# Performance work log

Measured on AMD Instinct MI355X. Metric: run time of the kernel, lower is better.

The kernel has to match this reference:

```python
import jax, jax.numpy as jnp
import numpy as np

INPUT_SIZE = 128
HID = 64
B, T = 256, 1024

def setup_inputs() -> dict:
    key = jax.random.key(0)
    ks = jax.random.split(key, 12)
    s1 = 1.0 / np.sqrt(HID)
    def u(k, shape):
        return jax.random.uniform(k, shape, jnp.float32, -s1, s1)
    return {
        "x": jax.random.normal(ks[0], (B, T, INPUT_SIZE), jnp.float32),
        "w_ih0": u(ks[1], (4 * HID, INPUT_SIZE)),
        "w_hh0": u(ks[2], (4 * HID, HID)),
        "b_ih0": u(ks[3], (4 * HID,)),
        "b_hh0": u(ks[4], (4 * HID,)),
        "w_ih1": u(ks[5], (4 * HID, HID)),
        "w_hh1": u(ks[6], (4 * HID, HID)),
        "b_ih1": u(ks[7], (4 * HID,)),
        "b_hh1": u(ks[8], (4 * HID,)),
        "w_out": u(ks[9], (1, HID)),
        "b_out": u(ks[10], (1,)),
    }

def _lstm(x, w_ih, w_hh, b_ih, b_hh):
    # x: [B, T, I] -> h sequence [B, T, H]; PyTorch gate order i, f, g, o
    Bb = x.shape[0]
    H = w_hh.shape[1]
    # precompute input contribution for all timesteps (one big GEMM)
    xg = jnp.einsum('bti,gi->btg', x, w_ih) + b_ih + b_hh  # [B, T, 4H]
    def step(carry, g_t):
        h, c = carry
        g = g_t + h @ w_hh.T  # [B, 4H]
        i, f, gg, o = jnp.split(g, 4, axis=-1)
        i = jax.nn.sigmoid(i)
        f = jax.nn.sigmoid(f)
        gg = jnp.tanh(gg)
        o = jax.nn.sigmoid(o)
        c = f * c + i * gg
        h = o * jnp.tanh(c)
        return (h, c), h
    init = (jnp.zeros((Bb, H), x.dtype), jnp.zeros((Bb, H), x.dtype))
    _, hs = jax.lax.scan(step, init, jnp.swapaxes(xg, 0, 1))  # [T, B, H]
    return jnp.swapaxes(hs, 0, 1)

def reference(x, w_ih0, w_hh0, b_ih0, b_hh0, w_ih1, w_hh1, b_ih1, b_hh1, w_out, b_out):
    h1 = _lstm(x, w_ih0, w_hh0, b_ih0, b_hh0)   # [B, T, H]
    h2 = _lstm(h1, w_ih1, w_hh1, b_ih1, b_hh1)  # [B, T, H]
    logits = jnp.einsum('bth,oh->bto', h2, w_out) + b_out  # [B, T, 1]
    return jax.nn.sigmoid(logits)
```

## Files before the change

kernel.cpp:

```cpp
#include <hip/hip_runtime.h>

#define BB 256
#define TT 1024
#define II 128
#define HH 64
#define BT (BB * TT)

typedef _Float16 h2 __attribute__((ext_vector_type(2)));
typedef _Float16 half8 __attribute__((ext_vector_type(8)));
typedef float f32x4 __attribute__((ext_vector_type(4)));
typedef unsigned int uint;
typedef unsigned short ushort;

#define DOT2(a, b, c) __builtin_amdgcn_fdot2((a), (b), (c), false)
#define BC(u) __builtin_bit_cast(h2, (uint)(u))
#define MFMA16(a, b, c) __builtin_amdgcn_mfma_f32_16x16x32_f16((a), (b), (c), 0, 0, 0)
#define SIG(v) __builtin_amdgcn_rcpf(1.0f + __expf(-(v)))
#define TNH(v) (1.0f - 2.0f * __builtin_amdgcn_rcpf(1.0f + __expf(2.0f * (v))))

#define BAR_W8() asm volatile("s_waitcnt lgkmcnt(8)\n\ts_barrier" ::: "memory")
#define BAR_W0() asm volatile("s_waitcnt lgkmcnt(0)\n\ts_barrier" ::: "memory")
#define BAR_NP() asm volatile("s_barrier" ::: "memory")

#define LDPK(P, ptr) uint P; { float2 _f = *(const float2*)(ptr); \
    h2 _h; _h[0] = (_Float16)_f.x; _h[1] = (_Float16)_f.y; \
    P = __builtin_bit_cast(uint, _h); }
#define PIN8(a,b,c,d,e,f,g,h_) asm volatile("" : "+v"(a),"+v"(b),"+v"(c),"+v"(d),"+v"(e),"+v"(f),"+v"(g),"+v"(h_));
#define LD8(P, base, o) \
    LDPK(P##0,(base)+(o)+ 0) LDPK(P##1,(base)+(o)+ 2) LDPK(P##2,(base)+(o)+ 4) LDPK(P##3,(base)+(o)+ 6) \
    LDPK(P##4,(base)+(o)+ 8) LDPK(P##5,(base)+(o)+10) LDPK(P##6,(base)+(o)+12) LDPK(P##7,(base)+(o)+14) \
    PIN8(P##0,P##1,P##2,P##3,P##4,P##5,P##6,P##7)

#define D8A(P, va, vb, c0, c1, c2, c3) \
    c0 = DOT2(BC(P##0), BC((va).x), c0); c1 = DOT2(BC(P##1), BC((va).y), c1); \
    c2 = DOT2(BC(P##2), BC((va).z), c2); c3 = DOT2(BC(P##3), BC((va).w), c3); \
    c0 = DOT2(BC(P##4), BC((vb).x), c0); c1 = DOT2(BC(P##5), BC((vb).y), c1); \
    c2 = DOT2(BC(P##6), BC((vb).z), c2); c3 = DOT2(BC(P##7), BC((vb).w), c3);

#define GDOT(G, s) { float a0=0.f,a1=0.f,a2=0.f,a3=0.f; \
    D8A(G##A, hv0, hv1, a0,a1,a2,a3) D8A(G##B, hv2, hv3, a0,a1,a2,a3) \
    D8A(G##C, hv4, hv5, a0,a1,a2,a3) D8A(G##D, hv6, hv7, a0,a1,a2,a3) \
    s = (a0 + a1) + (a2 + a3); }

#define LDHV(src) { const uint4* hq_ = (const uint4*)(src); \
    hv0=hq_[0]; hv1=hq_[1]; hv2=hq_[2]; hv3=hq_[3]; \
    hv4=hq_[4]; hv5=hq_[5]; hv6=hq_[6]; hv7=hq_[7]; }

__global__ __launch_bounds__(256)
void xg_mfma(const float* __restrict__ x, const float* __restrict__ w_ih0,
             ushort* __restrict__ xg)
{
    __shared__ __align__(16) _Float16 xt[64][136];
    __shared__ __align__(16) _Float16 wt[128][136];
    const int tid = threadIdx.x, lane = tid & 63, wv = tid >> 6;
    const int bt0 = blockIdx.x * 64;
    {
        const int row = tid >> 2, q = (tid & 3) * 32;
        const float4* src = (const float4*)(x + (size_t)(bt0 + row) * II + q);
        _Float16* dst = &xt[row][q];
        #pragma unroll
        for (int i = 0; i < 8; ++i) {
            float4 v = src[i];
            dst[4*i+0]=(_Float16)v.x; dst[4*i+1]=(_Float16)v.y;
            dst[4*i+2]=(_Float16)v.z; dst[4*i+3]=(_Float16)v.w;
        }
    }
    for (int nh = 0; nh < 2; ++nh) {
        __syncthreads();
        {
            const int n = tid >> 1, kh = (tid & 1) * 64;
            const int flatn = nh * 128 + n;
            const int srcrow = (flatn & 3) * 64 + (flatn >> 2);
            const float4* src = (const float4*)(w_ih0 + (size_t)srcrow * II + kh);
            _Float16* dst = &wt[n][kh];
            #pragma unroll
            for (int i = 0; i < 16; ++i) {
                float4 v = src[i];
                dst[4*i+0]=(_Float16)v.x; dst[4*i+1]=(_Float16)v.y;
                dst[4*i+2]=(_Float16)v.z; dst[4*i+3]=(_Float16)v.w;
            }
        }
        __syncthreads();
        const int m = wv * 16 + (lane & 15);
        const int kf = (lane >> 4) * 8;
        half8 a0 = *(const half8*)&xt[m][ 0 + kf];
        half8 a1 = *(const half8*)&xt[m][32 + kf];
        half8 a2 = *(const half8*)&xt[m][64 + kf];
        half8 a3 = *(const half8*)&xt[m][96 + kf];
        #pragma unroll
        for (int nt = 0; nt < 8; ++nt) {
            const int nloc = nt * 16 + (lane & 15);
            half8 b0 = *(const half8*)&wt[nloc][ 0 + kf];
            half8 b1 = *(const half8*)&wt[nloc][32 + kf];
            half8 b2 = *(const half8*)&wt[nloc][64 + kf];
            half8 b3 = *(const half8*)&wt[nloc][96 + kf];
            f32x4 acc = {0.f, 0.f, 0.f, 0.f};
            acc = MFMA16(a0, b0, acc); acc = MFMA16(a1, b1, acc);
            acc = MFMA16(a2, b2, acc); acc = MFMA16(a3, b3, acc);
            const int colg = nh * 128 + nt * 16 + (lane & 15);
            const int r0   = wv * 16 + (lane >> 4) * 4;
            #pragma unroll
            for (int r = 0; r < 4; ++r) {
                _Float16 hv = (_Float16)acc[r];
                xg[(size_t)(bt0 + r0 + r) * 256 + colg] = __builtin_bit_cast(ushort, hv);
            }
        }
    }
}

__global__ __launch_bounds__(192) __attribute__((amdgpu_waves_per_eu(1, 1)))
void lstm2_core(const float* __restrict__ w_hh0,
                const float* __restrict__ b_ih0, const float* __restrict__ b_hh0,
                const float* __restrict__ w_ih1, const float* __restrict__ w_hh1,
                const float* __restrict__ b_ih1, const float* __restrict__ b_hh1,
                const ushort* __restrict__ xg, ushort* __restrict__ h1g)
{
    const int bb = blockIdx.x;
    const int w  = threadIdx.x >> 6;
    const int j  = threadIdx.x & 63;

    __shared__ __align__(16) uint  h0buf[4][32];
    __shared__ __align__(16) uint  h1buf[32];
    __shared__ __align__(16) float zbuf[4][64][4];

    const float* Wsel = (w == 0) ? w_hh0 : (w == 1) ? w_ih1 : w_hh1;
    const float* r0p = Wsel + (size_t)(  0 + j) * 64;
    const float* r1p = Wsel + (size_t)( 64 + j) * 64;
    const float* r2p = Wsel + (size_t)(128 + j) * 64;
    const float* r3p = Wsel + (size_t)(192 + j) * 64;
    LD8(G0A, r0p,  0) LD8(G0B, r0p, 16) LD8(G0C, r0p, 32) LD8(G0D, r0p, 48)
    LD8(G1A, r1p,  0) LD8(G1B, r1p, 16) LD8(G1C, r1p, 32) LD8(G1D, r1p, 48)
    LD8(G2A, r2p,  0) LD8(G2B, r2p, 16) LD8(G2C, r2p, 32) LD8(G2D, r2p, 48)
    LD8(G3A, r3p,  0) LD8(G3B, r3p, 16) LD8(G3C, r3p, 32) LD8(G3D, r3p, 48)

    float bI = 0.f, bF = 0.f, bG = 0.f, bO = 0.f;
    if (w == 0) {
        bI = b_ih0[j]       + b_hh0[j];
        bF = b_ih0[64 + j]  + b_hh0[64 + j];
        bG = b_ih0[128 + j] + b_hh0[128 + j];
        bO = b_ih0[192 + j] + b_hh0[192 + j];
    } else if (w == 2) {
        bI = b_ih1[j]       + b_hh1[j];
        bF = b_ih1[64 + j]  + b_hh1[64 + j];
        bG = b_ih1[128 + j] + b_hh1[128 + j];
        bO = b_ih1[192 + j] + b_hh1[192 + j];
    }

    float cst = 0.0f;
    const ushort* xbase = xg + (size_t)bb * TT * 256 + j * 4;
    ushort* h1b = h1g + (size_t)bb * TT * 64 + j;

    uint4 hv0={0,0,0,0}, hv1={0,0,0,0}, hv2={0,0,0,0}, hv3={0,0,0,0};
    uint4 hv4={0,0,0,0}, hv5={0,0,0,0}, hv6={0,0,0,0}, hv7={0,0,0,0};
    f32x4 zr = {0.f, 0.f, 0.f, 0.f};
    uint2 xc = {0,0}, xn1 = {0,0}, xn2 = {0,0};
    if (w == 0) {
        xc  = *(const uint2*)(xbase);
        xn1 = *(const uint2*)(xbase + 256);
    }

    for (int k = 0; k < TT + 4; ++k) {
        if (w == 0) {
            if (k + 2 < TT) xn2 = *(const uint2*)(xbase + (size_t)(k + 2) * 256);
            if (k < TT) {
                float si, sf, sg, so;
                GDOT(G0, si) GDOT(G1, sf) GDOT(G2, sg) GDOT(G3, so)
                h2 xlo = BC(xc.x), xhi = BC(xc.y);
                si += bI + (float)xlo[0]; sf += bF + (float)xlo[1];
                sg += bG + (float)xhi[0]; so += bO + (float)xhi[1];
                float ii = SIG(si), ff = SIG(sf), gg = TNH(sg), oo = SIG(so);
                cst = fmaf(ff, cst, ii * gg);
                float hval = oo * TNH(cst);
                ((_Float16*)&h0buf[k & 3][0])[j] = (_Float16)hval;
                LDHV(&h0buf[k & 3][0]);
            }
            xc = xn1; xn1 = xn2;
            BAR_W8();
        } else if (w == 1) {
            if (k >= 2 && k < TT + 2) {
                const int m = k - 2;
                float si, sf, sg, so;
                GDOT(G0, si) GDOT(G1, sf) GDOT(G2, sg) GDOT(G3, so)
                f32x4 zv = {si, sf, sg, so};
                *(f32x4*)&zbuf[m & 3][j][0] = zv;
            }
            if (k >= 1 && k <= TT)
                LDHV(&h0buf[(k - 1) & 3][0]);
            BAR_W0();
        } else {
            if (k >= 4) {
                const int m = k - 4;
                float si, sf, sg, so;
                GDOT(G0, si) GDOT(G1, sf) GDOT(G2, sg) GDOT(G3, so)
                si += bI + zr[0]; sf += bF + zr[1];
                sg += bG + zr[2]; so += bO + zr[3];
                float ii = SIG(si), ff = SIG(sf), gg = TNH(sg), oo = SIG(so);
                cst = fmaf(ff, cst, ii * gg);
                float hval = oo * TNH(cst);
                _Float16 hf = (_Float16)hval;
                ((_Float16*)&h1buf[0])[j] = hf;
                LDHV(&h1buf[0]);
                h1b[(size_t)m * 64] = __builtin_bit_cast(ushort, hf);
            }
            if (k >= 3 && k < TT + 3)
                zr = *(const f32x4*)&zbuf[(k - 3) & 3][j][0];
            BAR_NP();
        }
    }
}

__global__ __launch_bounds__(256)
void head_gemv(const ushort* __restrict__ h1g, const float* __restrict__ w_out,
               const float* __restrict__ b_out, float* __restrict__ outp)
{
    __shared__ float wsh[64];
    const int tid = threadIdx.x;
    if (tid < 64) wsh[tid] = w_out[tid];
    __syncthreads();
    const int bt = blockIdx.x * 256 + tid;
    const uint4* hp = (const uint4*)(h1g + (size_t)bt * 64);
    float s = 0.0f;
    #pragma unroll
    for (int i = 0; i < 8; ++i) {
        uint4 v = hp[i];
        const float* wp = &wsh[8 * i];
        h2 p;
        p = BC(v.x); s = fmaf((float)p[0], wp[0], s); s = fmaf((float)p[1], wp[1], s);
        p = BC(v.y); s = fmaf((float)p[0], wp[2], s); s = fmaf((float)p[1], wp[3], s);
        p = BC(v.z); s = fmaf((float)p[0], wp[4], s); s = fmaf((float)p[1], wp[5], s);
        p = BC(v.w); s = fmaf((float)p[0], wp[6], s); s = fmaf((float)p[1], wp[7], s);
    }
    outp[bt] = __builtin_amdgcn_rcpf(1.0f + __expf(-(s + b_out[0])));
}

extern "C" void kernel_launch(void* const* d_in, const int* in_sizes, int n_in,
                              void* d_out, int out_size, void* d_ws, size_t ws_size,
                              hipStream_t stream) {
    const float* x     = (const float*)d_in[0];
    const float* w_ih0 = (const float*)d_in[1];
    const float* w_hh0 = (const float*)d_in[2];
    const float* b_ih0 = (const float*)d_in[3];
    const float* b_hh0 = (const float*)d_in[4];
    const float* w_ih1 = (const float*)d_in[5];
    const float* w_hh1 = (const float*)d_in[6];
    const float* b_ih1 = (const float*)d_in[7];
    const float* b_hh1 = (const float*)d_in[8];
    const float* w_out = (const float*)d_in[9];
    const float* b_out = (const float*)d_in[10];
    float* out = (float*)d_out;

    ushort* xg  = (ushort*)d_ws;
    ushort* h1g = (ushort*)((char*)d_ws + (size_t)BT * 256 * 2);

    hipLaunchKernelGGL(xg_mfma, dim3(BT / 64), dim3(256), 0, stream, x, w_ih0, xg);
    hipLaunchKernelGGL(lstm2_core, dim3(BB), dim3(192), 0, stream,
                       w_hh0, b_ih0, b_hh0, w_ih1, w_hh1, b_ih1, b_hh1, xg, h1g);
    hipLaunchKernelGGL(head_gemv, dim3(BT / 256), dim3(256), 0, stream,
                       h1g, w_out, b_out, out);
}
```

Before: 838.2 us.

## Process two timesteps per barrier and store gate inputs time-contiguous per unit

The recurrent kernel now advances two timesteps between workgroup barriers. The wave-specialized pipeline gets deeper staging, with lag offsets 3/6 and 8-entry LDS rings, so the three waves still hand off correctly. The precomputed input-gate tensor is written in a [batch][unit][time][gate] layout, which lets wave 0 fetch two timesteps with one 16-byte load. The aim is to halve barrier synchronization per step and make the input loads coalesced, at the cost of a uniform full lgkmcnt wait, more pipeline latency and scattered writes in the GEMM epilogue.

```diff
diff --git a/kernel.cpp b/kernel.cpp
--- a/kernel.cpp
+++ b/kernel.cpp
@@ -18,9 +18,7 @@
 #define SIG(v) __builtin_amdgcn_rcpf(1.0f + __expf(-(v)))
 #define TNH(v) (1.0f - 2.0f * __builtin_amdgcn_rcpf(1.0f + __expf(2.0f * (v))))
 
-#define BAR_W8() asm volatile("s_waitcnt lgkmcnt(8)\n\ts_barrier" ::: "memory")
-#define BAR_W0() asm volatile("s_waitcnt lgkmcnt(0)\n\ts_barrier" ::: "memory")
-#define BAR_NP() asm volatile("s_barrier" ::: "memory")
+#define BAR() asm volatile("s_waitcnt lgkmcnt(0)\n\ts_barrier" ::: "memory")
 
 #define LDPK(P, ptr) uint P; { float2 _f = *(const float2*)(ptr); \
     h2 _h; _h[0] = (_Float16)_f.x; _h[1] = (_Float16)_f.y; \
@@ -98,11 +96,15 @@
             acc = MFMA16(a0, b0, acc); acc = MFMA16(a1, b1, acc);
             acc = MFMA16(a2, b2, acc); acc = MFMA16(a3, b3, acc);
             const int colg = nh * 128 + nt * 16 + (lane & 15);
-            const int r0   = wv * 16 + (lane >> 4) * 4;
+            const int jj = colg >> 2, gg = colg & 3;
+            const int r0 = wv * 16 + (lane >> 4) * 4;
+            const int bloc = bt0 >> 10;
+            const int tb = (bt0 & 1023) + r0;
+            ushort* dst = xg + ((size_t)(bloc * 64 + jj) << 12) + gg;
             #pragma unroll
             for (int r = 0; r < 4; ++r) {
                 _Float16 hv = (_Float16)acc[r];
-                xg[(size_t)(bt0 + r0 + r) * 256 + colg] = __builtin_bit_cast(ushort, hv);
+                dst[(size_t)(tb + r) * 4] = __builtin_bit_cast(ushort, hv);
             }
         }
     }
@@ -119,9 +121,9 @@
     const int w  = threadIdx.x >> 6;
     const int j  = threadIdx.x & 63;
 
-    __shared__ __align__(16) uint  h0buf[4][32];
+    __shared__ __align__(16) uint  h0buf[8][32];
     __shared__ __align__(16) uint  h1buf[32];
-    __shared__ __align__(16) float zbuf[4][64][4];
+    __shared__ __align__(16) float zbuf[8][64][4];
 
     const float* Wsel = (w == 0) ? w_hh0 : (w == 1) ? w_ih1 : w_hh1;
     const float* r0p = Wsel + (size_t)(  0 + j) * 64;
@@ -147,66 +149,79 @@
     }
 
     float cst = 0.0f;
-    const ushort* xbase = xg + (size_t)bb * TT * 256 + j * 4;
+    const ushort* xb = xg + ((size_t)(bb * 64 + j) << 12);
     ushort* h1b = h1g + (size_t)bb * TT * 64 + j;
 
     uint4 hv0={0,0,0,0}, hv1={0,0,0,0}, hv2={0,0,0,0}, hv3={0,0,0,0};
     uint4 hv4={0,0,0,0}, hv5={0,0,0,0}, hv6={0,0,0,0}, hv7={0,0,0,0};
     f32x4 zr = {0.f, 0.f, 0.f, 0.f};
-    uint2 xc = {0,0}, xn1 = {0,0}, xn2 = {0,0};
+    uint4 q0 = {0,0,0,0}, q1 = {0,0,0,0};
     if (w == 0) {
-        xc  = *(const uint2*)(xbase);
-        xn1 = *(const uint2*)(xbase + 256);
-    }
-
-    for (int k = 0; k < TT + 4; ++k) {
+        q0 = *(const uint4*)(xb);
+        q1 = *(const uint4*)(xb + 8);
+    }
+
+#define PSTEP(KK, XLO, XHI) \
+    if ((KK) < TT) { \
+        float si, sf, sg, so; \
+        GDOT(G0, si) GDOT(G1, sf) GDOT(G2, sg) GDOT(G3, so) \
+        h2 xlo = BC(XLO), xhi = BC(XHI); \
+        si += bI + (float)xlo[0]; sf += bF + (float)xlo[1]; \
+        sg += bG + (float)xhi[0]; so += bO + (float)xhi[1]; \
+        float ii = SIG(si), ff = SIG(sf), gg = TNH(sg), oo = SIG(so); \
+        cst = fmaf(ff, cst, ii * gg); \
+        float hval = oo * TNH(cst); \
+        ((_Float16*)&h0buf[(KK) & 7][0])[j] = (_Float16)hval; \
+        LDHV(&h0buf[(KK) & 7][0]); \
+    }
+
+#define Q1STEP(KK) { const int i_ = (KK); \
+    if (i_ >= 3 && i_ < TT + 3) { \
+        const int m_ = i_ - 3; \
+        float si, sf, sg, so; \
+        GDOT(G0, si) GDOT(G1, sf) GDOT(G2, sg) GDOT(G3, so) \
+        f32x4 zv = {si, sf, sg, so}; \
+        *(f32x4*)&zbuf[m_ & 7][j][0] = zv; \
+    } \
+    if (i_ >= 2 && i_ < TT + 2) LDHV(&h0buf[(i_ - 2) & 7][0]) }
+
+#define Q2STEP(KK) { const int i_ = (KK); \
+    if (i_ >= 6) { \
+        const int m_ = i_ - 6; \
+        float si, sf, sg, so; \
+        GDOT(G0, si) GDOT(G1, sf) GDOT(G2, sg) GDOT(G3, so) \
+        si += bI + zr[0]; sf += bF + zr[1]; \
+        sg += bG + zr[2]; so += bO + zr[3]; \
+        float ii = SIG(si), ff = SIG(sf), gg = TNH(sg), oo = SIG(so); \
+        cst = fmaf(ff, cst, ii * gg); \
+        float hval = oo * TNH(cst); \
+        _Float16 hf = (_Float16)hval; \
+        ((_Float16*)&h1buf[0])[j] = hf; \
+        LDHV(&h1buf[0]); \
+        h1b[(size_t)m_ * 64] = __builtin_bit_cast(ushort, hf); \
+    } \
+    if (i_ >= 5 && i_ < TT + 5) zr = *(const f32x4*)&zbuf[(i_ - 5) & 7][j][0]; }
+
+    for (int k0 = 0; k0 < TT + 6; k0 += 2) {
         if (w == 0) {
-            if (k + 2 < TT) xn2 = *(const uint2*)(xbase + (size_t)(k + 2) * 256);
-            if (k < TT) {
-                float si, sf, sg, so;
-                GDOT(G0, si) GDOT(G1, sf) GDOT(G2, sg) GDOT(G3, so)
-                h2 xlo = BC(xc.x), xhi = BC(xc.y);
-                si += bI + (float)xlo[0]; sf += bF + (float)xlo[1];
-                sg += bG + (float)xhi[0]; so += bO + (float)xhi[1];
-                float ii = SIG(si), ff = SIG(sf), gg = TNH(sg), oo = SIG(so);
-                cst = fmaf(ff, cst, ii * gg);
-                float hval = oo * TNH(cst);
-                ((_Float16*)&h0buf[k & 3][0])[j] = (_Float16)hval;
-                LDHV(&h0buf[k & 3][0]);
-            }
-            xc = xn1; xn1 = xn2;
-            BAR_W8();
+            uint4 qn = q1;
+            if (k0 + 4 < TT)
+                qn = *(const uint4*)(xb + (size_t)(k0 + 4) * 4);
+            PSTEP(k0,     q0.x, q0.y)
+            PSTEP(k0 + 1, q0.z, q0.w)
+            q0 = q1; q1 = qn;
         } else if (w == 1) {
-            if (k >= 2 && k < TT + 2) {
-                const int m = k - 2;
-                float si, sf, sg, so;
-                GDOT(G0, si) GDOT(G1, sf) GDOT(G2, sg) GDOT(G3, so)
-                f32x4 zv = {si, sf, sg, so};
-                *(f32x4*)&zbuf[m & 3][j][0] = zv;
-            }
-            if (k >= 1 && k <= TT)
-                LDHV(&h0buf[(k - 1) & 3][0]);
-            BAR_W0();
+            Q1STEP(k0)
+            Q1STEP(k0 + 1)
         } else {
-            if (k >= 4) {
-                const int m = k - 4;
-                float si, sf, sg, so;
-                GDOT(G0, si) GDOT(G1, sf) GDOT(G2, sg) GDOT(G3, so)
-                si += bI + zr[0]; sf += bF + zr[1];
-                sg += bG + zr[2]; so += bO + zr[3];
-                float ii = SIG(si), ff = SIG(sf), gg = TNH(sg), oo = SIG(so);
-                cst = fmaf(ff, cst, ii * gg);
-                float hval = oo * TNH(cst);
-                _Float16 hf = (_Float16)hval;
-                ((_Float16*)&h1buf[0])[j] = hf;
-                LDHV(&h1buf[0]);
-                h1b[(size_t)m * 64] = __builtin_bit_cast(ushort, hf);
-            }
-            if (k >= 3 && k < TT + 3)
-                zr = *(const f32x4*)&zbuf[(k - 3) & 3][j][0];
-            BAR_NP();
-        }
-    }
+            Q2STEP(k0)
+            Q2STEP(k0 + 1)
+        }
+        BAR();
+    }
+#undef PSTEP
+#undef Q1STEP
+#undef Q2STEP
 }
 
 __global__ __launch_bounds__(256)
```

Result: faster. 811.3 us (-3.2%).
